# Kernel tuning notes

Hardware: AMD Instinct MI355X
Metric: run time of the kernel (lower is better)

Reference implementation:

```python
import jax, jax.numpy as jnp
import numpy as np

OUT_H, OUT_W = 7, 7
SR = 2            # sampling_ratio
SCALE = 0.25      # spatial_scale


def setup_inputs() -> dict:
    key = jax.random.key(0)
    k1, k2, k3, k4, k5 = jax.random.split(key, 5)
    inp = jax.random.normal(k1, (2, 256, 200, 200), dtype=jnp.float32)
    K = 512
    cx = jax.random.uniform(k2, (K,), minval=100.0, maxval=700.0)
    cy = jax.random.uniform(k3, (K,), minval=100.0, maxval=700.0)
    wh = jax.random.uniform(k4, (K, 2), minval=32.0, maxval=192.0)
    x1 = jnp.clip(cx - wh[:, 0] / 2, 0.0, 798.0)
    x2 = jnp.clip(cx + wh[:, 0] / 2, x1 + 1.0, 800.0)
    y1 = jnp.clip(cy - wh[:, 1] / 2, 0.0, 798.0)
    y2 = jnp.clip(cy + wh[:, 1] / 2, y1 + 1.0, 800.0)
    bi = jax.random.randint(k5, (K,), 0, 2).astype(jnp.float32)
    rois = jnp.stack([bi, x1, y1, x2, y2], axis=1).astype(jnp.float32)
    return {"input": inp, "rois": rois}


def _sample_coords(start, bin_size, pooled, sr):
    # bin-major sample ordering: [bin0_s0, bin0_s1, bin1_s0, ...] as in the torch code
    p = jnp.arange(pooled, dtype=jnp.float32)
    i = jnp.arange(sr, dtype=jnp.float32)
    grid = bin_size[:, None, None] * p[None, :, None] \
         + (bin_size / sr)[:, None, None] * (i + 0.5)[None, None, :]
    K = start.shape[0]
    return start[:, None] + grid.reshape(K, pooled * sr)  # [K, pooled*sr]


def _roi_align(input, rois):
    H, W = input.shape[2], input.shape[3]
    K, C = rois.shape[0], input.shape[1]
    b = rois[:, 0].astype(jnp.int32)
    x1, y1, x2, y2 = (rois[:, j] * SCALE for j in (1, 2, 3, 4))
    roi_w = jnp.maximum(x2 - x1, 1.0)
    roi_h = jnp.maximum(y2 - y1, 1.0)
    y = _sample_coords(y1, roi_h / OUT_H, OUT_H, SR)  # [K, OUT_H*SR]
    x = _sample_coords(x1, roi_w / OUT_W, OUT_W, SR)  # [K, OUT_W*SR]
    # original zeroes an entire ROI if any sample falls outside [-1, H] x [-1, W]
    valid = jnp.all((y >= -1.0) & (y <= H), axis=1) & \
            jnp.all((x >= -1.0) & (x <= W), axis=1)   # [K]
    yc = jnp.clip(y, 0.0, H - 1.0)
    xc = jnp.clip(x, 0.0, W - 1.0)
    yl = jnp.floor(yc)
    xl = jnp.floor(xc)
    yh = jnp.clip(yl + 1.0, 0.0, H - 1.0)
    xh = jnp.clip(xl + 1.0, 0.0, W - 1.0)
    ly = yc - yl
    lx = xc - xl
    hy = 1.0 - ly
    hx = 1.0 - lx
    yl_i, yh_i = yl.astype(jnp.int32), yh.astype(jnp.int32)
    xl_i, xh_i = xl.astype(jnp.int32), xh.astype(jnp.int32)
    bi = b[:, None, None]  # [K,1,1]

    def gather(yi, xi):
        # mixed advanced indexing -> [K, Sy, Sx, C]
        return input[bi, :, yi[:, :, None], xi[:, None, :]]

    v1 = gather(yl_i, xl_i)
    v2 = gather(yl_i, xh_i)
    v3 = gather(yh_i, xl_i)
    v4 = gather(yh_i, xh_i)
    w1 = hy[:, :, None] * hx[:, None, :]
    w2 = hy[:, :, None] * lx[:, None, :]
    w3 = ly[:, :, None] * hx[:, None, :]
    w4 = ly[:, :, None] * lx[:, None, :]
    res = (w1[..., None] * v1 + w2[..., None] * v2 +
           w3[..., None] * v3 + w4[..., None] * v4)  # [K, Sy, Sx, C]
    # average SRxSR samples per bin; original hardcodes division by 4 (== SR*SR here)
    res = res.reshape(K, OUT_H, SR, OUT_W, SR, C).sum(axis=(2, 4)) / 4.0
    res = res * valid[:, None, None, None].astype(res.dtype)
    return jnp.transpose(res, (0, 3, 1, 2))  # [K, C, OUT_H, OUT_W]


def reference(input, rois):
    return _roi_align(input, rois)
```

## Files before the change

### kernel.cpp

```cpp
#include <hip/hip_runtime.h>

#define IN_H 200
#define IN_W 200
#define NCH  256
#define NROI 512
#define OUT_HW 49
#define PLANE (IN_H * IN_W)

__global__ __launch_bounds__(256) void transpose_bf16_kernel(
    const float* __restrict__ in, ushort* __restrict__ nhwc) {
  __shared__ ushort t[64][260];
  const int blk = blockIdx.x;
  const int hwt = blk % 625;
  const int b   = blk / 625;
  const int w = threadIdx.x >> 6, l = threadIdx.x & 63;
  const int hw0 = hwt * 64;

  const float* src = in + (size_t)b * NCH * PLANE + hw0;
#pragma unroll 4
  for (int i = 0; i < 64; ++i) {
    const int c = w * 64 + i;
    const float v = src[(size_t)c * PLANE + l];
    const unsigned u = __float_as_uint(v);
    const unsigned r = (u + 0x7fffu + ((u >> 16) & 1u)) >> 16;
    t[l][c] = (ushort)r;
  }
  __syncthreads();

  ushort* dst = nhwc + ((size_t)b * PLANE + hw0) * NCH;
#pragma unroll
  for (int m = threadIdx.x; m < 64 * 64; m += 256) {
    const int h = m >> 6;
    const int q = m & 63;
    *(ushort4*)(dst + (size_t)h * NCH + q * 4) = *(const ushort4*)&t[h][q * 4];
  }
}

__device__ inline void acc8(float* acc, uint4 q, float w) {
  acc[0] += w * __uint_as_float(q.x << 16);
  acc[1] += w * __uint_as_float(q.x & 0xffff0000u);
  acc[2] += w * __uint_as_float(q.y << 16);
  acc[3] += w * __uint_as_float(q.y & 0xffff0000u);
  acc[4] += w * __uint_as_float(q.z << 16);
  acc[5] += w * __uint_as_float(q.z & 0xffff0000u);
  acc[6] += w * __uint_as_float(q.w << 16);
  acc[7] += w * __uint_as_float(q.w & 0xffff0000u);
}

__global__ __launch_bounds__(256) void roi_nhwc_bf16_kernel(
    const ushort* __restrict__ nhwc,
    const float* __restrict__ rois,
    float* __restrict__ out) {
  __shared__ float sout[128 * OUT_HW];

  const int blk  = blockIdx.x;
  const int k    = blk >> 1;
  const int half = blk & 1;
  const int t    = threadIdx.x;
  const int pg   = t >> 4;
  const int cl   = (t & 15) * 8;
  const int c0   = half * 128 + cl;

  const float* r = rois + k * 5;
  const int   b   = (int)r[0];
  const float x1s = r[1] * 0.25f;
  const float y1s = r[2] * 0.25f;
  const float x2s = r[3] * 0.25f;
  const float y2s = r[4] * 0.25f;
  const float roi_w = fmaxf(x2s - x1s, 1.0f);
  const float roi_h = fmaxf(y2s - y1s, 1.0f);
  const float bw = roi_w / 7.0f;
  const float bh = roi_h / 7.0f;

  const bool valid = (y1s + 0.25f * bh >= -1.0f) && (y1s + 6.75f * bh <= (float)IN_H) &&
                     (x1s + 0.25f * bw >= -1.0f) && (x1s + 6.75f * bw <= (float)IN_W);
  const float scale = valid ? 0.25f : 0.0f;

  const ushort* base = nhwc + (size_t)b * PLANE * NCH + c0;

  for (int p = pg; p < OUT_HW; p += 16) {
    const int ph = p / 7;
    const int pw = p - ph * 7;
    const float ybase = y1s + bh * (float)ph;
    const float xbase = x1s + bw * (float)pw;

    float acc[8] = {0.f, 0.f, 0.f, 0.f, 0.f, 0.f, 0.f, 0.f};
#pragma unroll
    for (int iy = 0; iy < 2; ++iy) {
      const float y  = ybase + (bh * 0.5f) * ((float)iy + 0.5f);
      const float yc = fminf(fmaxf(y, 0.0f), (float)(IN_H - 1));
      const float ylf = floorf(yc);
      const int   yl  = (int)ylf;
      const int   yh  = min(yl + 1, IN_H - 1);
      const float ly  = yc - ylf;
      const float hy  = 1.0f - ly;
      const ushort* rowl = base + (size_t)yl * IN_W * NCH;
      const ushort* rowh = base + (size_t)yh * IN_W * NCH;
#pragma unroll
      for (int ix = 0; ix < 2; ++ix) {
        const float x  = xbase + (bw * 0.5f) * ((float)ix + 0.5f);
        const float xc = fminf(fmaxf(x, 0.0f), (float)(IN_W - 1));
        const float xlf = floorf(xc);
        const int   xl  = (int)xlf;
        const int   xh  = min(xl + 1, IN_W - 1);
        const float lx  = xc - xlf;
        const float hx  = 1.0f - lx;

        const uint4 q1 = *(const uint4*)(rowl + (size_t)xl * NCH);
        const uint4 q2 = *(const uint4*)(rowl + (size_t)xh * NCH);
        const uint4 q3 = *(const uint4*)(rowh + (size_t)xl * NCH);
        const uint4 q4 = *(const uint4*)(rowh + (size_t)xh * NCH);

        acc8(acc, q1, hy * hx);
        acc8(acc, q2, hy * lx);
        acc8(acc, q3, ly * hx);
        acc8(acc, q4, ly * lx);
      }
    }
#pragma unroll
    for (int j = 0; j < 8; ++j) sout[(cl + j) * OUT_HW + p] = acc[j] * scale;
  }
  __syncthreads();

  float4* o4 = (float4*)(out + ((size_t)k * NCH + half * 128) * OUT_HW);
  const float4* s4 = (const float4*)sout;
  for (int m = t; m < (128 * OUT_HW) / 4; m += 256) o4[m] = s4[m];
}

__global__ __launch_bounds__(256) void roi_align_fallback(
    const float* __restrict__ input,
    const float* __restrict__ rois,
    float* __restrict__ out) {
  const int blk  = blockIdx.x;
  const int k    = blk >> 6;
  const int cg   = blk & 63;
  const int wave = threadIdx.x >> 6;
  const int lane = threadIdx.x & 63;
  const int c    = (cg << 2) + wave;

  const float* r = rois + k * 5;
  const int   b   = (int)r[0];
  const float x1s = r[1] * 0.25f;
  const float y1s = r[2] * 0.25f;
  const float roi_w = fmaxf(r[3] * 0.25f - x1s, 1.0f);
  const float roi_h = fmaxf(r[4] * 0.25f - y1s, 1.0f);
  const float bw = roi_w / 7.0f;
  const float bh = roi_h / 7.0f;
  const bool valid = (y1s + 0.25f * bh >= -1.0f) && (y1s + 6.75f * bh <= (float)IN_H) &&
                     (x1s + 0.25f * bw >= -1.0f) && (x1s + 6.75f * bw <= (float)IN_W);
  if (lane >= OUT_HW) return;
  const int ph = lane / 7;
  const int pw = lane - ph * 7;
  const float* plane = input + ((size_t)(b * NCH + c)) * PLANE;
  const float ybase = y1s + bh * (float)ph;
  const float xbase = x1s + bw * (float)pw;
  float acc = 0.0f;
#pragma unroll
  for (int iy = 0; iy < 2; ++iy) {
    const float y  = ybase + (bh * 0.5f) * ((float)iy + 0.5f);
    const float yc = fminf(fmaxf(y, 0.0f), (float)(IN_H - 1));
    const float ylf = floorf(yc);
    const int yl = (int)ylf;
    const int yh = min(yl + 1, IN_H - 1);
    const float ly = yc - ylf, hy = 1.0f - ly;
#pragma unroll
    for (int ix = 0; ix < 2; ++ix) {
      const float x  = xbase + (bw * 0.5f) * ((float)ix + 0.5f);
      const float xc = fminf(fmaxf(x, 0.0f), (float)(IN_W - 1));
      const float xlf = floorf(xc);
      const int xl = (int)xlf;
      const int xh = min(xl + 1, IN_W - 1);
      const float lx = xc - xlf, hx = 1.0f - lx;
      const float* row_l = plane + yl * IN_W;
      const float* row_h = plane + yh * IN_W;
      acc += hy * hx * row_l[xl] + hy * lx * row_l[xh] +
             ly * hx * row_h[xl] + ly * lx * row_h[xh];
    }
  }
  out[((size_t)k * NCH + c) * OUT_HW + lane] = valid ? acc * 0.25f : 0.0f;
}

extern "C" void kernel_launch(void* const* d_in, const int* in_sizes, int n_in,
                              void* d_out, int out_size, void* d_ws, size_t ws_size,
                              hipStream_t stream) {
  const float* input = (const float*)d_in[0];
  const float* rois  = (const float*)d_in[1];
  float* out = (float*)d_out;

  const size_t need = (size_t)2 * PLANE * NCH * sizeof(ushort);
  if (ws_size >= need) {
    ushort* nhwc = (ushort*)d_ws;
    transpose_bf16_kernel<<<2 * 625, 256, 0, stream>>>(input, nhwc);
    roi_nhwc_bf16_kernel<<<NROI * 2, 256, 0, stream>>>(nhwc, rois, out);
  } else {
    roi_align_fallback<<<NROI * (NCH / 4), 256, 0, stream>>>(input, rois, out);
  }
}
```

Measured before the change: 44.72 us.

## Pipeline per-batch transpose with ROI sampling across three staged launches

Splits the work into three launches. The first transposes batch 0 to NHWC bf16. The second transposes batch 1 while, in the same grid, it runs the ROI blocks whose ROIs belong to batch 0. The third runs the ROIs for batch 1. The goal is to overlap ROI gather work with the transpose traffic instead of serialising the two. In exchange it adds a third launch and many early-exiting blocks, since every ROI block is launched twice but only one copy does the work.

```diff
diff --git a/kernel.cpp b/kernel.cpp
--- a/kernel.cpp
+++ b/kernel.cpp
@@ -6,35 +6,7 @@
 #define NROI 512
 #define OUT_HW 49
 #define PLANE (IN_H * IN_W)
-
-__global__ __launch_bounds__(256) void transpose_bf16_kernel(
-    const float* __restrict__ in, ushort* __restrict__ nhwc) {
-  __shared__ ushort t[64][260];
-  const int blk = blockIdx.x;
-  const int hwt = blk % 625;
-  const int b   = blk / 625;
-  const int w = threadIdx.x >> 6, l = threadIdx.x & 63;
-  const int hw0 = hwt * 64;
-
-  const float* src = in + (size_t)b * NCH * PLANE + hw0;
-#pragma unroll 4
-  for (int i = 0; i < 64; ++i) {
-    const int c = w * 64 + i;
-    const float v = src[(size_t)c * PLANE + l];
-    const unsigned u = __float_as_uint(v);
-    const unsigned r = (u + 0x7fffu + ((u >> 16) & 1u)) >> 16;
-    t[l][c] = (ushort)r;
-  }
-  __syncthreads();
-
-  ushort* dst = nhwc + ((size_t)b * PLANE + hw0) * NCH;
-#pragma unroll
-  for (int m = threadIdx.x; m < 64 * 64; m += 256) {
-    const int h = m >> 6;
-    const int q = m & 63;
-    *(ushort4*)(dst + (size_t)h * NCH + q * 4) = *(const ushort4*)&t[h][q * 4];
-  }
-}
+#define NTILE_B 625
 
 __device__ inline void acc8(float* acc, uint4 q, float w) {
   acc[0] += w * __uint_as_float(q.x << 16);
@@ -47,22 +19,59 @@
   acc[7] += w * __uint_as_float(q.w & 0xffff0000u);
 }
 
-__global__ __launch_bounds__(256) void roi_nhwc_bf16_kernel(
-    const ushort* __restrict__ nhwc,
+union ShMem {
+  ushort t[64][260];
+  float  sout[128 * OUT_HW];
+};
+
+template <int PHASE>
+__global__ __launch_bounds__(256) void stage_kernel(
+    const float* __restrict__ in,
     const float* __restrict__ rois,
+    ushort* __restrict__ nhwc,
     float* __restrict__ out) {
-  __shared__ float sout[128 * OUT_HW];
-
-  const int blk  = blockIdx.x;
-  const int k    = blk >> 1;
-  const int half = blk & 1;
-  const int t    = threadIdx.x;
-  const int pg   = t >> 4;
-  const int cl   = (t & 15) * 8;
-  const int c0   = half * 128 + cl;
+  __shared__ ShMem sh;
+  const int bid = blockIdx.x;
+  const int tid = threadIdx.x;
+
+  if (PHASE == 0 || (PHASE == 1 && bid < NTILE_B)) {
+    const int tb  = (PHASE == 0) ? 0 : 1;
+    const int hwt = bid;
+    const int hw0 = hwt * 64;
+    const int w = tid >> 6, l = tid & 63;
+
+    const float* src = in + (size_t)tb * NCH * PLANE + hw0;
+#pragma unroll 4
+    for (int i = 0; i < 64; ++i) {
+      const int c = w * 64 + i;
+      const float v = src[(size_t)c * PLANE + l];
+      const unsigned u = __float_as_uint(v);
+      const unsigned rr = (u + 0x7fffu + ((u >> 16) & 1u)) >> 16;
+      sh.t[l][c] = (ushort)rr;
+    }
+    __syncthreads();
+    ushort* dst = nhwc + ((size_t)tb * PLANE + hw0) * NCH;
+    for (int m = tid; m < 64 * 64; m += 256) {
+      const int h = m >> 6;
+      const int q = m & 63;
+      *(ushort4*)(dst + (size_t)h * NCH + q * 4) = *(const ushort4*)&sh.t[h][q * 4];
+    }
+    return;
+  }
+
+  const int slot = (PHASE == 1) ? (bid - NTILE_B) : bid;
+  const int k    = slot >> 1;
+  const int half = slot & 1;
 
   const float* r = rois + k * 5;
-  const int   b   = (int)r[0];
+  const int rb = (int)r[0];
+  if (PHASE == 1) { if (rb != 0) return; }
+  else            { if (rb != 1) return; }
+
+  const int pg = tid >> 4;
+  const int cl = (tid & 15) * 8;
+  const int c0 = half * 128 + cl;
+
   const float x1s = r[1] * 0.25f;
   const float y1s = r[2] * 0.25f;
   const float x2s = r[3] * 0.25f;
@@ -76,7 +85,7 @@
                      (x1s + 0.25f * bw >= -1.0f) && (x1s + 6.75f * bw <= (float)IN_W);
   const float scale = valid ? 0.25f : 0.0f;
 
-  const ushort* base = nhwc + (size_t)b * PLANE * NCH + c0;
+  const ushort* base = nhwc + (size_t)rb * PLANE * NCH + c0;
 
   for (int p = pg; p < OUT_HW; p += 16) {
     const int ph = p / 7;
@@ -118,13 +127,13 @@
       }
     }
 #pragma unroll
-    for (int j = 0; j < 8; ++j) sout[(cl + j) * OUT_HW + p] = acc[j] * scale;
+    for (int j = 0; j < 8; ++j) sh.sout[(cl + j) * OUT_HW + p] = acc[j] * scale;
   }
   __syncthreads();
 
   float4* o4 = (float4*)(out + ((size_t)k * NCH + half * 128) * OUT_HW);
-  const float4* s4 = (const float4*)sout;
-  for (int m = t; m < (128 * OUT_HW) / 4; m += 256) o4[m] = s4[m];
+  const float4* s4 = (const float4*)sh.sout;
+  for (int m = tid; m < (128 * OUT_HW) / 4; m += 256) o4[m] = s4[m];
 }
 
 __global__ __launch_bounds__(256) void roi_align_fallback(
@@ -190,8 +199,9 @@
   const size_t need = (size_t)2 * PLANE * NCH * sizeof(ushort);
   if (ws_size >= need) {
     ushort* nhwc = (ushort*)d_ws;
-    transpose_bf16_kernel<<<2 * 625, 256, 0, stream>>>(input, nhwc);
-    roi_nhwc_bf16_kernel<<<NROI * 2, 256, 0, stream>>>(nhwc, rois, out);
+    stage_kernel<0><<<NTILE_B, 256, 0, stream>>>(input, rois, nhwc, out);
+    stage_kernel<1><<<NTILE_B + 2 * NROI, 256, 0, stream>>>(input, rois, nhwc, out);
+    stage_kernel<2><<<2 * NROI, 256, 0, stream>>>(input, rois, nhwc, out);
   } else {
     roi_align_fallback<<<NROI * (NCH / 4), 256, 0, stream>>>(input, rois, out);
   }
```

After: 52.87 us. 1.18x slower.
